# Optimization experiments

Measured on AMD Instinct MI355X. Metric: run time of the kernel, lower is better.

## Reference

```python
import jax, jax.numpy as jnp
import numpy as np

EPS = 1e-08

def log_g(x):
    return jnp.log(jnp.tanh(x) + EPS)

def parallel_scan(log_coeffs, log_values):
    # log_coeffs: [B, L, H], log_values: [B, L+1, H]
    a_star = jnp.pad(jnp.cumsum(log_coeffs, axis=1), ((0, 0), (1, 0), (0, 0)))
    log_h0_plus_b_star = jax.lax.cumlogsumexp(log_values - a_star, axis=1)
    log_h = a_star + log_h0_plus_b_star
    return jnp.exp(log_h)[:, 1:, :]

def setup_inputs() -> dict:
    key = jax.random.key(0)
    B, L, I, H, O = 16, 4096, 64, 512, 1
    ks = jax.random.split(key, 8)
    s_i = 1.0 / np.sqrt(I)
    s_h = 1.0 / np.sqrt(H)
    return {
        "x": jax.random.normal(ks[0], (B, L, I), dtype=jnp.float32),
        "Wz0": jax.random.uniform(ks[1], (I, H), jnp.float32, -s_i, s_i),
        "bz0": jnp.zeros((H,), jnp.float32),
        "Wh0": jax.random.uniform(ks[2], (I, H), jnp.float32, -s_i, s_i),
        "bh0": jnp.zeros((H,), jnp.float32),
        "Wz1": jax.random.uniform(ks[3], (H, H), jnp.float32, -s_h, s_h),
        "bz1": jnp.zeros((H,), jnp.float32),
        "Wh1": jax.random.uniform(ks[4], (H, H), jnp.float32, -s_h, s_h),
        "bh1": jnp.zeros((H,), jnp.float32),
        "Wf": jax.random.uniform(ks[5], (H, O), jnp.float32, -s_h, s_h),
        "bf": jnp.zeros((O,), jnp.float32),
    }

def min_gru_layer(inp, Wz, bz, Wh, bh):
    B, L, _ = inp.shape
    H = Wz.shape[1]
    k = jax.nn.sigmoid(inp @ Wz + bz)          # [B, L, H]
    log_z = -jax.nn.softplus(-k)               # (faithful: softplus of sigmoid output)
    log_coeffs = -jax.nn.softplus(k)
    log_h0 = jnp.full((B, 1, H), jnp.log(EPS), dtype=inp.dtype)  # log_g(zeros)
    log_h_wavy = log_g(jax.nn.sigmoid(inp @ Wh + bh))
    log_values = jnp.concatenate([log_h0, log_z + log_h_wavy], axis=1)  # [B, L+1, H]
    return parallel_scan(log_coeffs, log_values)

def reference(x, Wz0, bz0, Wh0, bh0, Wz1, bz1, Wh1, bh1, Wf, bf):
    h = min_gru_layer(x, Wz0, bz0, Wh0, bh0)
    h = min_gru_layer(h, Wz1, bz1, Wh1, bh1)
    return h[:, -1, :] @ Wf + bf  # [B, output_size]
```

## Files before the change

### kernel.cpp

```cpp
#include <hip/hip_runtime.h>
#include <hip/hip_fp16.h>

#define EPSF 1e-8f

typedef _Float16 half8 __attribute__((ext_vector_type(8)));
typedef float f32x4 __attribute__((ext_vector_type(4)));


__device__ __forceinline__ float fast_rcp(float x) {
    return __builtin_amdgcn_rcpf(x);
}
__device__ __forceinline__ void gate_transform(float pz, float ph, float& a, float& b) {
    float ez = __expf(-pz);
    float k  = fast_rcp(1.0f + ez);
    float ek = __expf(-k);
    float z  = fast_rcp(1.0f + ek);
    a = ek * z;
    float es = __expf(-ph);
    float s  = fast_rcp(1.0f + es);
    float e2 = __expf(-2.0f * s);
    float hw = (1.0f - e2) * fast_rcp(1.0f + e2) + EPSF;
    b = z * hw;
}

__device__ __forceinline__ void gload16(const void* g, void* l) {
    __builtin_amdgcn_global_load_lds(
        (const __attribute__((address_space(1))) unsigned int*)g,
        (__attribute__((address_space(3))) unsigned int*)l, 16, 0, 0);
}

__device__ __forceinline__ void qscan(int q, float pA, float pB,
                                      float& fA, float& fB, float& prA, float& prB)
{
    float oA = __shfl_xor(pA, 16, 64), oB = __shfl_xor(pB, 16, 64);
    float eA = (q & 1) ? oA : pA, eB = (q & 1) ? oB : pB;
    float lA = (q & 1) ? pA : oA, lB = (q & 1) ? pB : oB;
    float p2A = eA * lA;
    float p2B = fmaf(lA, eB, lB);
    float o2A = __shfl_xor(p2A, 32, 64), o2B = __shfl_xor(p2B, 32, 64);
    float loA = (q & 2) ? o2A : p2A, loB = (q & 2) ? o2B : p2B;
    float hiA = (q & 2) ? p2A : o2A, hiB = (q & 2) ? p2B : o2B;
    fA = loA * hiA;
    fB = fmaf(hiA, loB, hiB);
    prA = (q & 2) ? o2A : 1.0f;
    prB = (q & 2) ? o2B : 0.0f;
    if (q & 1) { prB = fmaf(oA, prB, oB); prA *= oA; }
}

__global__ __launch_bounds__(256) void kprep(
    const float* __restrict__ Wz1, const float* __restrict__ Wh1,
    __half* __restrict__ Wtz1, __half* __restrict__ Wth1,
    const float* __restrict__ Wz0, const float* __restrict__ Wh0,
    __half* __restrict__ Wtz0, __half* __restrict__ Wth0,
    const float* __restrict__ bf, float* __restrict__ out)
{
    __shared__ float t[64][65];
    const int tid = threadIdx.x;
    int b = blockIdx.x;
    if (b == 0 && tid < 16) out[tid] = bf[0];
    const float* W; __half* Wt; int ldt, n0, k0;
    if (b < 64)       { W = Wz1; Wt = Wtz1; ldt = 512; n0 = (b & 7) * 64; k0 = (b >> 3) * 64; }
    else if (b < 128) { b -= 64;  W = Wh1; Wt = Wth1; ldt = 512; n0 = (b & 7) * 64; k0 = (b >> 3) * 64; }
    else if (b < 136) { b -= 128; W = Wz0; Wt = Wtz0; ldt = 64;  n0 = b * 64; k0 = 0; }
    else              { b -= 136; W = Wh0; Wt = Wth0; ldt = 64;  n0 = b * 64; k0 = 0; }
    const int r = tid >> 4, c4 = (tid & 15) * 4;
#pragma unroll
    for (int rr = 0; rr < 64; rr += 16)
        *(float4*)&t[rr + r][c4] = *(const float4*)&W[(size_t)(k0 + rr + r) * 512 + n0 + c4];
    __syncthreads();
#pragma unroll
    for (int rr = 0; rr < 64; rr += 16) {
        const int row = rr + r;
        __half2 h01 = __floats2half2_rn(t[c4 + 0][row], t[c4 + 1][row]);
        __half2 h23 = __floats2half2_rn(t[c4 + 2][row], t[c4 + 3][row]);
        *(__half2*)&Wt[(size_t)(n0 + row) * ldt + k0 + c4] = h01;
        *(__half2*)&Wt[(size_t)(n0 + row) * ldt + k0 + c4 + 2] = h23;
    }
}

__global__ __launch_bounds__(256) void k1s(
    const float* __restrict__ x,
    const __half* __restrict__ Wtz, const __half* __restrict__ Wth,
    const float* __restrict__ bz, const float* __restrict__ bh,
    __half* __restrict__ h0red)
{
    __shared__ char smem1[32768];
    __half* As = (__half*)smem1;
    __half* Bs = As + 128 * 64;
    float* carray = (float*)(smem1 + 16384);
    __half* h0s = (__half*)smem1;
    const int tid = threadIdx.x;
    const int wave = tid >> 6, lane = tid & 63;
    const int q = lane >> 4, l16 = lane & 15;
    const int wm = wave >> 1, wn = wave & 1;

    const int bx = blockIdx.x, by = blockIdx.y;
    const int n0 = bx * 64;
    const float* xsrc = x + (size_t)by * 262144 + 253952;

    {
        const int r8 = lane >> 3, ch = lane & 7;
#pragma unroll
        for (int i = 0; i < 4; ++i) {
            const int reg = wave * 4 + i;
            const int row = reg * 8 + r8;
            const __half* src = (row < 64) ? (Wtz + (size_t)(n0 + row) * 64)
                                           : (Wth + (size_t)(n0 + row - 64) * 64);
            gload16(src + ((ch ^ (row & 7)) << 3), (char*)Bs + reg * 1024);
        }
#pragma unroll
        for (int i = 0; i < 4; ++i) {
            const int reg = wave * 4 + i;
            const int row = reg * 8 + r8;
            const int c0 = (ch ^ (row & 7)) * 8;
            float4 v0 = *(const float4*)(xsrc + row * 64 + c0);
            float4 v1 = *(const float4*)(xsrc + row * 64 + c0 + 4);
            __half2* dst = (__half2*)((char*)As + reg * 1024 + lane * 16);
            dst[0] = __floats2half2_rn(v0.x, v0.y);
            dst[1] = __floats2half2_rn(v0.z, v0.w);
            dst[2] = __floats2half2_rn(v1.x, v1.y);
            dst[3] = __floats2half2_rn(v1.z, v1.w);
        }
    }
    __syncthreads();

    f32x4 accz[4][2], acch[4][2];
#pragma unroll
    for (int mi = 0; mi < 4; ++mi)
#pragma unroll
        for (int ni = 0; ni < 2; ++ni) {
            accz[mi][ni] = (f32x4){0.f, 0.f, 0.f, 0.f};
            acch[mi][ni] = (f32x4){0.f, 0.f, 0.f, 0.f};
        }

#pragma unroll
    for (int s = 0; s < 2; ++s) {
        half8 af[4];
#pragma unroll
        for (int mi = 0; mi < 4; ++mi) {
            const int row = wm * 64 + mi * 16 + l16;
            const int pc = (s * 4 + q) ^ (row & 7);
            af[mi] = *(const half8*)&As[row * 64 + pc * 8];
        }
#pragma unroll
        for (int ni = 0; ni < 2; ++ni) {
            const int rn = wn * 32 + ni * 16 + l16;
            const int pc = (s * 4 + q) ^ (rn & 7);
            half8 bzf = *(const half8*)&Bs[rn * 64 + pc * 8];
            half8 bhf = *(const half8*)&Bs[(64 + rn) * 64 + pc * 8];
#pragma unroll
            for (int mi = 0; mi < 4; ++mi) {
                accz[mi][ni] = __builtin_amdgcn_mfma_f32_16x16x32_f16(af[mi], bzf, accz[mi][ni], 0, 0, 0);
                acch[mi][ni] = __builtin_amdgcn_mfma_f32_16x16x32_f16(af[mi], bhf, acch[mi][ni], 0, 0, 0);
            }
        }
    }

    float rB[2];
    if (wm == 0) {
#pragma unroll
        for (int ni = 0; ni < 2; ++ni) {
            const int col = n0 + wn * 32 + ni * 16 + l16;
            const float bzv = bz[col], bhv = bh[col];
            float runA = 1.f, runB = 0.f;
#pragma unroll
            for (int mi = 0; mi < 4; ++mi) {
                float av[4], bv[4], pA = 1.f, pB = 0.f;
#pragma unroll
                for (int j = 0; j < 4; ++j) {
                    gate_transform(accz[mi][ni][j] + bzv, acch[mi][ni][j] + bhv, av[j], bv[j]);
                    pB = fmaf(av[j], pB, bv[j]); pA *= av[j];
                }
                float fA, fB, prA, prB;
                qscan(q, pA, pB, fA, fB, prA, prB);
                runB = fmaf(fA, runB, fB); runA *= fA;
            }
            rB[ni] = runB;
        }
    }
    __syncthreads();
    if (wm == 0 && q == 0) {
#pragma unroll
        for (int ni = 0; ni < 2; ++ni)
            carray[wn * 32 + ni * 16 + l16] = rB[ni];
    }
    __syncthreads();
    if (wm == 1) {
#pragma unroll
        for (int ni = 0; ni < 2; ++ni) {
            const int colloc = wn * 32 + ni * 16 + l16;
            const int col = n0 + colloc;
            const float bzv = bz[col], bhv = bh[col];
            float H = carray[colloc];
#pragma unroll
            for (int mi = 0; mi < 4; ++mi) {
                float av[4], bv[4], pA = 1.f, pB = 0.f;
#pragma unroll
                for (int j = 0; j < 4; ++j) {
                    gate_transform(accz[mi][ni][j] + bzv, acch[mi][ni][j] + bhv, av[j], bv[j]);
                    pB = fmaf(av[j], pB, bv[j]); pA *= av[j];
                }
                float fA, fB, prA, prB;
                qscan(q, pA, pB, fA, fB, prA, prB);
                float Hl = fmaf(prA, H, prB);
                const int rloc = mi * 16 + q * 4;
#pragma unroll
                for (int j = 0; j < 4; ++j) {
                    Hl = fmaf(av[j], Hl, bv[j]);
                    h0s[(rloc + j) * 68 + colloc] = (__half)Hl;
                }
                H = fmaf(fA, H, fB);
            }
        }
    }
    __syncthreads();
    {
        const int row = tid >> 2, cpart = tid & 3;
        const __half* srcp = h0s + row * 68 + cpart * 16;
        __half* dstp = h0red + (size_t)(by * 64 + row) * 512 + n0 + cpart * 16;
        *(uint4*)dstp = *(const uint4*)srcp;
        *(uint4*)(dstp + 8) = *(const uint4*)(srcp + 8);
    }
}

__global__ __launch_bounds__(256, 2) void k4_l1(
    const __half* __restrict__ h0red,
    const __half* __restrict__ Wtz, const __half* __restrict__ Wth,
    const float* __restrict__ bz, const float* __restrict__ bh,
    const float* __restrict__ Wf, float* __restrict__ out)
{
    __shared__ char smem4[2][24576];
    const int tid = threadIdx.x;
    const int wave = tid >> 6, lane = tid & 63;
    const int q = lane >> 4, l16 = lane & 15;
    const int wm = wave >> 1, wn = wave & 1;

    const int bx = blockIdx.x, by = blockIdx.y;
    const int m0 = by * 128, n0 = bx * 128;

    const int r4 = lane >> 2, ch = lane & 3;

    const __half* aSrc[2]; int aDst[2];
#pragma unroll
    for (int i = 0; i < 2; ++i) {
        const int reg = wave * 2 + i;
        const int row = reg * 16 + r4;
        const int pc = ch ^ ((row >> 1) & 3);
        aSrc[i] = h0red + (size_t)(m0 + row) * 512 + pc * 8;
        aDst[i] = reg * 1024;
    }
    const __half* bSrc[4]; int bDst[4];
#pragma unroll
    for (int i = 0; i < 4; ++i) {
        const int reg = wave * 4 + i;
        const int row = reg * 16 + r4;
        const int pc = ch ^ ((row >> 1) & 3);
        bSrc[i] = ((row < 128) ? (Wtz + (size_t)(n0 + row) * 512)
                               : (Wth + (size_t)(n0 + row - 128) * 512)) + pc * 8;
        bDst[i] = 8192 + reg * 1024;
    }
    int aOff[4], bOff[4];
#pragma unroll
    for (int mi = 0; mi < 4; ++mi) {
        const int row = wm * 64 + mi * 16 + l16;
        aOff[mi] = row * 64 + ((q ^ ((row >> 1) & 3)) << 4);
    }
#pragma unroll
    for (int ni = 0; ni < 4; ++ni) {
        const int rn = wn * 64 + ni * 16 + l16;
        bOff[ni] = 8192 + rn * 64 + ((q ^ ((rn >> 1) & 3)) << 4);
    }

    f32x4 accz[4][4], acch[4][4];
#pragma unroll
    for (int mi = 0; mi < 4; ++mi)
#pragma unroll
        for (int ni = 0; ni < 4; ++ni) {
            accz[mi][ni] = (f32x4){0.f, 0.f, 0.f, 0.f};
            acch[mi][ni] = (f32x4){0.f, 0.f, 0.f, 0.f};
        }

    auto stage = [&](int c, int t) {
#pragma unroll
        for (int i = 0; i < 2; ++i)
            gload16(aSrc[i] + t * 32, smem4[c] + aDst[i]);
#pragma unroll
        for (int i = 0; i < 4; ++i)
            gload16(bSrc[i] + t * 32, smem4[c] + bDst[i]);
    };
    auto compute = [&](int c) {
        half8 af[4];
#pragma unroll
        for (int mi = 0; mi < 4; ++mi)
            af[mi] = *(const half8*)(smem4[c] + aOff[mi]);
        __builtin_amdgcn_s_setprio(1);
#pragma unroll
        for (int ni = 0; ni < 4; ++ni) {
            half8 bzf = *(const half8*)(smem4[c] + bOff[ni]);
            half8 bhf = *(const half8*)(smem4[c] + 8192 + bOff[ni]);
#pragma unroll
            for (int mi = 0; mi < 4; ++mi) {
                accz[mi][ni] = __builtin_amdgcn_mfma_f32_16x16x32_f16(af[mi], bzf, accz[mi][ni], 0, 0, 0);
                acch[mi][ni] = __builtin_amdgcn_mfma_f32_16x16x32_f16(af[mi], bhf, acch[mi][ni], 0, 0, 0);
            }
        }
        __builtin_amdgcn_s_setprio(0);
    };

    stage(0, 0);
#pragma unroll
    for (int t = 0; t < 15; ++t) {
        const int c = t & 1;
        stage(c ^ 1, t + 1);
        asm volatile("s_waitcnt vmcnt(6)" ::: "memory");
        __builtin_amdgcn_s_barrier();
        compute(c);
        __builtin_amdgcn_s_barrier();
    }
    asm volatile("s_waitcnt vmcnt(0)" ::: "memory");
    __builtin_amdgcn_s_barrier();
    compute(1);

    const int batch = by * 2 + wm;
    float part = 0.f;
#pragma unroll
    for (int ni = 0; ni < 4; ++ni) {
        const int col = n0 + wn * 64 + ni * 16 + l16;
        const float bzv = bz[col], bhv = bh[col];
        float fullA = 1.f, fullB = 0.f;
#pragma unroll
        for (int mi = 0; mi < 4; ++mi) {
            float pA = 1.f, pB = 0.f;
#pragma unroll
            for (int j = 0; j < 4; ++j) {
                float a, b;
                gate_transform(accz[mi][ni][j] + bzv, acch[mi][ni][j] + bhv, a, b);
                pB = fmaf(a, pB, b); pA *= a;
            }
            float fA, fB, prA, prB;
            qscan(q, pA, pB, fA, fB, prA, prB);
            fullB = fmaf(fA, fullB, fB); fullA *= fA;
        }
        if (q == 0) part = fmaf(fullB, Wf[col], part);
    }
#pragma unroll
    for (int off = 32; off; off >>= 1) part += __shfl_down(part, off, 64);
    if (lane == 0) atomicAdd(&out[batch], part);
}

extern "C" void kernel_launch(void* const* d_in, const int* in_sizes, int n_in,
                              void* d_out, int out_size, void* d_ws, size_t ws_size,
                              hipStream_t stream)
{
    const float* x   = (const float*)d_in[0];
    const float* Wz0 = (const float*)d_in[1];
    const float* bz0 = (const float*)d_in[2];
    const float* Wh0 = (const float*)d_in[3];
    const float* bh0 = (const float*)d_in[4];
    const float* Wz1 = (const float*)d_in[5];
    const float* bz1 = (const float*)d_in[6];
    const float* Wh1 = (const float*)d_in[7];
    const float* bh1 = (const float*)d_in[8];
    const float* Wf  = (const float*)d_in[9];
    const float* bf  = (const float*)d_in[10];
    float* out = (float*)d_out;

    char* ws = (char*)d_ws;
    __half* h0red = (__half*)ws;
    __half* Wtz1  = (__half*)(ws + (1024 << 10));
    __half* Wth1  = Wtz1 + 262144;
    __half* Wtz0  = Wth1 + 262144;
    __half* Wth0  = Wtz0 + 32768;

    kprep<<<144, 256, 0, stream>>>(Wz1, Wh1, Wtz1, Wth1,
                                   Wz0, Wh0, Wtz0, Wth0, bf, out);
    k1s<<<dim3(8, 16), 256, 0, stream>>>(x, Wtz0, Wth0, bz0, bh0, h0red);
    k4_l1<<<dim3(4, 8), 256, 0, stream>>>(h0red, Wtz1, Wth1, bz1, bh1, Wf, out);
}
```

Baseline: 33.10 us.

## Fuse weight transpose/convert prep kernel into first-layer kernel

Removes the separate kprep launch. Each k1s block now transposes and converts one 64x64 tile of the layer-1 weights to fp16 for the later kernel. It also builds its own fp16 layer-0 weight tile in shared memory straight from the fp32 weights, and block 0 initializes the output with the bias. This saves one kernel launch and the round-trip through global memory for the layer-0 weights. In exchange, each block uses more shared memory and runs extra syncs and transpose work before its GEMM.

```diff
diff --git a/kernel.cpp b/kernel.cpp
--- a/kernel.cpp
+++ b/kernel.cpp
@@ -47,46 +47,19 @@
     if (q & 1) { prB = fmaf(oA, prB, oB); prA *= oA; }
 }
 
-__global__ __launch_bounds__(256) void kprep(
-    const float* __restrict__ Wz1, const float* __restrict__ Wh1,
-    __half* __restrict__ Wtz1, __half* __restrict__ Wth1,
-    const float* __restrict__ Wz0, const float* __restrict__ Wh0,
-    __half* __restrict__ Wtz0, __half* __restrict__ Wth0,
-    const float* __restrict__ bf, float* __restrict__ out)
-{
-    __shared__ float t[64][65];
-    const int tid = threadIdx.x;
-    int b = blockIdx.x;
-    if (b == 0 && tid < 16) out[tid] = bf[0];
-    const float* W; __half* Wt; int ldt, n0, k0;
-    if (b < 64)       { W = Wz1; Wt = Wtz1; ldt = 512; n0 = (b & 7) * 64; k0 = (b >> 3) * 64; }
-    else if (b < 128) { b -= 64;  W = Wh1; Wt = Wth1; ldt = 512; n0 = (b & 7) * 64; k0 = (b >> 3) * 64; }
-    else if (b < 136) { b -= 128; W = Wz0; Wt = Wtz0; ldt = 64;  n0 = b * 64; k0 = 0; }
-    else              { b -= 136; W = Wh0; Wt = Wth0; ldt = 64;  n0 = b * 64; k0 = 0; }
-    const int r = tid >> 4, c4 = (tid & 15) * 4;
-#pragma unroll
-    for (int rr = 0; rr < 64; rr += 16)
-        *(float4*)&t[rr + r][c4] = *(const float4*)&W[(size_t)(k0 + rr + r) * 512 + n0 + c4];
-    __syncthreads();
-#pragma unroll
-    for (int rr = 0; rr < 64; rr += 16) {
-        const int row = rr + r;
-        __half2 h01 = __floats2half2_rn(t[c4 + 0][row], t[c4 + 1][row]);
-        __half2 h23 = __floats2half2_rn(t[c4 + 2][row], t[c4 + 3][row]);
-        *(__half2*)&Wt[(size_t)(n0 + row) * ldt + k0 + c4] = h01;
-        *(__half2*)&Wt[(size_t)(n0 + row) * ldt + k0 + c4 + 2] = h23;
-    }
-}
-
 __global__ __launch_bounds__(256) void k1s(
     const float* __restrict__ x,
-    const __half* __restrict__ Wtz, const __half* __restrict__ Wth,
+    const float* __restrict__ Wz0, const float* __restrict__ Wh0,
+    const float* __restrict__ Wz1, const float* __restrict__ Wh1,
     const float* __restrict__ bz, const float* __restrict__ bh,
-    __half* __restrict__ h0red)
+    const float* __restrict__ bf,
+    __half* __restrict__ Wtz1, __half* __restrict__ Wth1,
+    __half* __restrict__ h0red, float* __restrict__ out)
 {
-    __shared__ char smem1[32768];
+    __shared__ char smem1[49408];
     __half* As = (__half*)smem1;
     __half* Bs = As + 128 * 64;
+    float (*t)[65] = (float(*)[65])(smem1 + 32768);
     float* carray = (float*)(smem1 + 16384);
     __half* h0s = (__half*)smem1;
     const int tid = threadIdx.x;
@@ -95,19 +68,14 @@
     const int wm = wave >> 1, wn = wave & 1;
 
     const int bx = blockIdx.x, by = blockIdx.y;
+    const int Lb = bx + 8 * by;
     const int n0 = bx * 64;
     const float* xsrc = x + (size_t)by * 262144 + 253952;
 
+    if (Lb == 0 && tid < 16) out[tid] = bf[0];
+
     {
         const int r8 = lane >> 3, ch = lane & 7;
-#pragma unroll
-        for (int i = 0; i < 4; ++i) {
-            const int reg = wave * 4 + i;
-            const int row = reg * 8 + r8;
-            const __half* src = (row < 64) ? (Wtz + (size_t)(n0 + row) * 64)
-                                           : (Wth + (size_t)(n0 + row - 64) * 64);
-            gload16(src + ((ch ^ (row & 7)) << 3), (char*)Bs + reg * 1024);
-        }
 #pragma unroll
         for (int i = 0; i < 4; ++i) {
             const int reg = wave * 4 + i;
@@ -120,6 +88,46 @@
             dst[1] = __floats2half2_rn(v0.z, v0.w);
             dst[2] = __floats2half2_rn(v1.x, v1.y);
             dst[3] = __floats2half2_rn(v1.z, v1.w);
+        }
+    }
+
+    const int r = tid >> 4, c4 = (tid & 15) * 4;
+    {
+        const int mat = Lb >> 6, ti = Lb & 63;
+        const int n0t = (ti & 7) * 64, k0t = (ti >> 3) * 64;
+        const float* W = mat ? Wh1 : Wz1;
+        __half* Wt = mat ? Wth1 : Wtz1;
+#pragma unroll
+        for (int rr = 0; rr < 64; rr += 16)
+            *(float4*)&t[rr + r][c4] = *(const float4*)&W[(size_t)(k0t + rr + r) * 512 + n0t + c4];
+        __syncthreads();
+#pragma unroll
+        for (int rr = 0; rr < 64; rr += 16) {
+            const int row = rr + r;
+            __half2 h01 = __floats2half2_rn(t[c4 + 0][row], t[c4 + 1][row]);
+            __half2 h23 = __floats2half2_rn(t[c4 + 2][row], t[c4 + 3][row]);
+            *(__half2*)&Wt[(size_t)(n0t + row) * 512 + k0t + c4] = h01;
+            *(__half2*)&Wt[(size_t)(n0t + row) * 512 + k0t + c4 + 2] = h23;
+        }
+    }
+    {
+        const int n = tid & 63, cw = (tid >> 6) * 2;
+#pragma unroll
+        for (int mat = 0; mat < 2; ++mat) {
+            const float* W = mat ? Wh0 : Wz0;
+            __syncthreads();
+#pragma unroll
+            for (int rr = 0; rr < 64; rr += 16)
+                *(float4*)&t[rr + r][c4] = *(const float4*)&W[(size_t)(rr + r) * 512 + n0 + c4];
+            __syncthreads();
+#pragma unroll
+            for (int cc = 0; cc < 2; ++cc) {
+                const int chunk = cw + cc;
+                half8 hv;
+#pragma unroll
+                for (int j = 0; j < 8; ++j) hv[j] = (_Float16)t[chunk * 8 + j][n];
+                *(half8*)&Bs[(mat * 64 + n) * 64 + ((chunk ^ (n & 7)) << 3)] = hv;
+            }
         }
     }
     __syncthreads();
@@ -369,11 +377,8 @@
     __half* h0red = (__half*)ws;
     __half* Wtz1  = (__half*)(ws + (1024 << 10));
     __half* Wth1  = Wtz1 + 262144;
-    __half* Wtz0  = Wth1 + 262144;
-    __half* Wth0  = Wtz0 + 32768;
-
-    kprep<<<144, 256, 0, stream>>>(Wz1, Wh1, Wtz1, Wth1,
-                                   Wz0, Wh0, Wtz0, Wth0, bf, out);
-    k1s<<<dim3(8, 16), 256, 0, stream>>>(x, Wtz0, Wth0, bz0, bh0, h0red);
+
+    k1s<<<dim3(8, 16), 256, 0, stream>>>(x, Wz0, Wh0, Wz1, Wh1, bz0, bh0, bf,
+                                         Wtz1, Wth1, h0red, out);
     k4_l1<<<dim3(4, 8), 256, 0, stream>>>(h0red, Wtz1, Wth1, bz1, bh1, Wf, out);
 }
```

Result: faster. 32.31 us, median of 2 (-2.4%).
